# Optimization experiments

Measured on AMD Instinct MI355X. Metric: run time of the kernel, lower is better.

Reference implementation:

```python
import jax, jax.numpy as jnp
import numpy as np

ROPE_DIMS = 16
NUM_HEADS = 16
NUM_KV_HEADS = 4
HEAD_DIM = 128
ROPE_BASE = 10000.0


def _rope_cos_sin(T, dtype):
    # inv_freq over rope_dims=16 -> 8 freqs; emb = cat(freqs, freqs) -> 16 cols
    inv_freq = 1.0 / (ROPE_BASE ** (jnp.arange(0, ROPE_DIMS, 2, dtype=jnp.float32) / ROPE_DIMS))
    t = jnp.arange(T, dtype=jnp.float32)
    freqs = jnp.outer(t, inv_freq)              # [T, 8]
    emb = jnp.concatenate([freqs, freqs], -1)   # [T, 16]
    return jnp.cos(emb).astype(dtype), jnp.sin(emb).astype(dtype)


def _apply_rotary(x):
    # x: [B, H, T, head_dim]; rotate only first ROPE_DIMS dims
    T = x.shape[-2]
    cos, sin = _rope_cos_sin(T, x.dtype)        # [T, 16]
    x_rope, x_pass = x[..., :ROPE_DIMS], x[..., ROPE_DIMS:]
    half = ROPE_DIMS // 2
    x1, x2 = x_rope[..., :half], x_rope[..., half:]
    rotated = jnp.concatenate([-x2, x1], -1)
    x_rope = x_rope * cos + rotated * sin
    return jnp.concatenate([x_rope, x_pass], -1)


def setup_inputs() -> dict:
    key = jax.random.key(0)
    ks = jax.random.split(key, 5)
    B, T, C = 4, 2048, 2048
    kv_out = NUM_KV_HEADS * HEAD_DIM
    s = 0.02
    return {
        "x_normed": jax.random.normal(ks[0], (B, T, C), jnp.float32),
        "q_w": jax.random.normal(ks[1], (C, C), jnp.float32) * s,
        "k_w": jax.random.normal(ks[2], (kv_out, C), jnp.float32) * s,
        "v_w": jax.random.normal(ks[3], (kv_out, C), jnp.float32) * s,
        "out_w": jax.random.normal(ks[4], (C, C), jnp.float32) * s,
        "qk_gain": jnp.ones((1, NUM_HEADS, 1, 1), jnp.float32),
    }


def reference(x_normed, q_w, k_w, v_w, out_w, qk_gain):
    B, T, C = x_normed.shape
    H, kvH, hd = NUM_HEADS, NUM_KV_HEADS, HEAD_DIM
    q = (x_normed @ q_w.T).reshape(B, T, H, hd).transpose(0, 2, 1, 3)    # [B,H,T,hd]
    k = (x_normed @ k_w.T).reshape(B, T, kvH, hd).transpose(0, 2, 1, 3)  # [B,kvH,T,hd]
    v = (x_normed @ v_w.T).reshape(B, T, kvH, hd).transpose(0, 2, 1, 3)
    q = _apply_rotary(q)
    k = _apply_rotary(k)
    q = q * qk_gain
    reps = H // kvH
    if reps > 1:
        k = jnp.repeat(k, reps, axis=1)  # [B,H,T,hd]
        v = jnp.repeat(v, reps, axis=1)
    scale = 1.0 / jnp.sqrt(jnp.asarray(hd, q.dtype))
    scores = jnp.einsum('bhqd,bhkd->bhqk', q, k) * scale
    causal = jnp.tril(jnp.ones((T, T), bool))
    scores = jnp.where(causal, scores, jnp.asarray(-jnp.inf, scores.dtype))
    probs = jax.nn.softmax(scores, axis=-1)
    attn = jnp.einsum('bhqk,bhkd->bhqd', probs, v)
    attn = attn.transpose(0, 2, 1, 3).reshape(B, T, C)
    out = attn @ out_w.T
    return out, v[:, :kvH]
```

## Files before the change

### kernel.cpp

```cpp
#include <hip/hip_runtime.h>
#include <hip/hip_bf16.h>
#include <stdint.h>
#include <math.h>

#define T_SEQ 2048
#define CDIM  2048
#define NB    4
#define NH    16
#define NKV   4
#define HD    128

typedef __attribute__((ext_vector_type(8))) short short8;
typedef __attribute__((ext_vector_type(4))) float f32x4;

__device__ __forceinline__ void gload_lds16(const void* g, void* l) {
  __builtin_amdgcn_global_load_lds((const __attribute__((address_space(1))) void*)g,
                                   (__attribute__((address_space(3))) void*)l, 16, 0, 0);
}

__device__ __forceinline__ f32x4 mfma_bf16(short8 a, short8 b, f32x4 c) {
  return __builtin_amdgcn_mfma_f32_16x16x32_bf16(a, b, c, 0, 0, 0);
}

__device__ __forceinline__ unsigned short f2bf(float x) {
  union { float f; unsigned u; } v; v.f = x;
  unsigned r = v.u + 0x7fffu + ((v.u >> 16) & 1u);
  return (unsigned short)(r >> 16);
}

__device__ __forceinline__ unsigned pk_bf16(float a, float b) {
  unsigned r;
  asm("v_cvt_pk_bf16_f32 %0, %1, %2" : "=v"(r) : "v"(a), "v"(b));
  return r;
}

__device__ __forceinline__ float exp2_fast(float x) {
  float r;
  asm("v_exp_f32 %0, %1" : "=v"(r) : "v"(x));
  return r;
}

__device__ __forceinline__ void barrier_hard() {
  __builtin_amdgcn_s_barrier();
  __builtin_amdgcn_sched_barrier(0);
}

__global__ void cvt_all(const float* __restrict__ x,  const float* __restrict__ qw,
                        const float* __restrict__ kw, const float* __restrict__ vw,
                        const float* __restrict__ ow,
                        unsigned short* __restrict__ xb,  unsigned short* __restrict__ qwb,
                        unsigned short* __restrict__ kwb, unsigned short* __restrict__ vwb,
                        unsigned short* __restrict__ owb) {
  const int bid = blockIdx.x;
  const float* src; unsigned short* dst; int base, nb, n4;
  if (bid < 2048)      { src = x;  dst = xb;  base = 0;    nb = 2048; n4 = 4194304; }
  else if (bid < 2560) { src = qw; dst = qwb; base = 2048; nb = 512;  n4 = 1048576; }
  else if (bid < 2688) { src = kw; dst = kwb; base = 2560; nb = 128;  n4 = 262144;  }
  else if (bid < 2816) { src = vw; dst = vwb; base = 2688; nb = 128;  n4 = 262144;  }
  else                 { src = ow; dst = owb; base = 2816; nb = 512;  n4 = 1048576; }
  const int stride = nb * 256;
  for (int i = (bid - base) * 256 + threadIdx.x; i < n4; i += stride) {
    float4 v = *(const float4*)(src + (size_t)i * 4);
    ushort4 o;
    o.x = f2bf(v.x); o.y = f2bf(v.y); o.z = f2bf(v.z); o.w = f2bf(v.w);
    *(ushort4*)(dst + (size_t)i * 4) = o;
  }
}

template<int MODE>
__launch_bounds__(512, 2)
__global__ void gemm256(const unsigned short* __restrict__ A,
                        const unsigned short* __restrict__ W,
                        int N, int K,
                        unsigned short* __restrict__ obf,
                        float* __restrict__ of32,
                        const float* __restrict__ gain)
{
  __shared__ alignas(16) short As[2][2][256 * 32];
  __shared__ alignas(16) short Bs[2][2][256 * 32];
  const int tid = threadIdx.x;
  const int lane = tid & 63, w = tid >> 6;
  const int wr = w >> 2, wc = w & 3;
  const int lr = lane & 15, lg = lane >> 4;

  const int nwg  = gridDim.x * gridDim.y;
  const int orig = blockIdx.y * gridDim.x + blockIdx.x;
  const int cpx  = nwg >> 3;
  const int swz  = (orig & 7) * cpx + (orig >> 3);
  const int m0 = (swz / gridDim.x) * 256, n0 = (swz % gridDim.x) * 256;

  f32x4 acc[8][4] = {};
  const int nkt = K >> 6;
  const int rsw = (lr >> 1) & 3;

  auto stageA = [&](int kt, int buf, int kk) {
#pragma unroll
    for (int i = 0; i < 2; ++i) {
      int t = i * 512 + tid;
      int row = t >> 2;
      int cs = (t & 3) ^ ((t >> 3) & 3);
      gload_lds16(A + (size_t)(m0 + row) * K + kt * 64 + kk * 32 + cs * 8,
                  (char*)&As[buf][kk][0] + i * 8192 + w * 1024);
    }
  };
  auto stageB = [&](int kt, int buf, int kk) {
#pragma unroll
    for (int i = 0; i < 2; ++i) {
      int t = i * 512 + tid;
      int row = t >> 2;
      int cs = (t & 3) ^ ((t >> 3) & 3);
      gload_lds16(W + (size_t)(n0 + row) * K + kt * 64 + kk * 32 + cs * 8,
                  (char*)&Bs[buf][kk][0] + i * 8192 + w * 1024);
    }
  };

  stageA(0, 0, 0); stageB(0, 0, 0); stageA(0, 0, 1); stageB(0, 0, 1);
  asm volatile("s_waitcnt vmcnt(4)" ::: "memory");
  __builtin_amdgcn_s_barrier();

  int cur = 0;
  for (int kt = 0; kt < nkt; ++kt) {
    const int tn = (kt + 1 < nkt) ? kt + 1 : kt;
#pragma unroll
    for (int kk = 0; kk < 2; ++kk) {
      short8 bfr[4], af[4];
#pragma unroll
      for (int fn = 0; fn < 4; ++fn) {
        int rb = wc * 64 + fn * 16 + lr;
        bfr[fn] = *(const short8*)((const char*)&Bs[cur][kk][0] + rb * 64 + ((lg ^ rsw) << 4));
      }
#pragma unroll
      for (int fm = 0; fm < 4; ++fm) {
        int ra = wr * 128 + fm * 16 + lr;
        af[fm] = *(const short8*)((const char*)&As[cur][kk][0] + ra * 64 + ((lg ^ rsw) << 4));
      }
      stageA(tn, cur ^ 1, kk);
      __builtin_amdgcn_s_barrier();
      __builtin_amdgcn_s_setprio(1);
#pragma unroll
      for (int fm = 0; fm < 4; ++fm)
#pragma unroll
        for (int fn = 0; fn < 4; ++fn)
          acc[fm][fn] = mfma_bf16(af[fm], bfr[fn], acc[fm][fn]);
      __builtin_amdgcn_s_setprio(0);
      __builtin_amdgcn_s_barrier();

#pragma unroll
      for (int fm = 0; fm < 4; ++fm) {
        int ra = wr * 128 + (4 + fm) * 16 + lr;
        af[fm] = *(const short8*)((const char*)&As[cur][kk][0] + ra * 64 + ((lg ^ rsw) << 4));
      }
      stageB(tn, cur ^ 1, kk);
      asm volatile("s_waitcnt vmcnt(4)" ::: "memory");
      __builtin_amdgcn_s_barrier();
      __builtin_amdgcn_s_setprio(1);
#pragma unroll
      for (int fm = 0; fm < 4; ++fm)
#pragma unroll
        for (int fn = 0; fn < 4; ++fn)
          acc[4 + fm][fn] = mfma_bf16(af[fm], bfr[fn], acc[4 + fm][fn]);
      __builtin_amdgcn_s_setprio(0);
      __builtin_amdgcn_s_barrier();
    }
    cur ^= 1;
  }
  asm volatile("s_waitcnt vmcnt(0)" ::: "memory");

#pragma unroll
  for (int fm = 0; fm < 8; ++fm) {
    const int mbase = m0 + wr * 128 + fm * 16 + lg * 4;
#pragma unroll
    for (int fn = 0; fn < 4; ++fn) {
      const int ncol = n0 + wc * 64 + fn * 16 + lr;
      if constexpr (MODE == 0) {
#pragma unroll
        for (int r = 0; r < 4; ++r)
          of32[(size_t)(mbase + r) * N + ncol] = acc[fm][fn][r];
      } else {
        const int hh = ncol >> 7;
        const int d  = ncol & 127;
        const bool rope = ((wc & 1) == 0) && (fn == 0);
#pragma unroll
        for (int r = 0; r < 4; ++r) {
          float val = acc[fm][fn][r];
          const int m  = mbase + r;
          const int t  = m & (T_SEQ - 1);
          const int bb = m >> 11;
          if (rope) {
            float partner = __shfl_xor(val, 8);
            float invf = exp2f(-(float)(d & 7) * 1.6609640474436813f);
            float ang = (float)t * invf;
            float sn, cn;
            sincosf(ang, &sn, &cn);
            float rot = (d < 8) ? -partner : partner;
            val = val * cn + rot * sn;
          }
          val *= gain[hh] * 0.12751742676f;
          obf[(size_t)((bb * NH + hh) * T_SEQ + t) * HD + d] = f2bf(val);
        }
      }
    }
  }
}

__launch_bounds__(256, 2)
__global__ void gemm_kv(const unsigned short* __restrict__ A,
                        const unsigned short* __restrict__ W,
                        unsigned short* __restrict__ Kout,
                        unsigned short* __restrict__ Vt,
                        float* __restrict__ vout)
{
  __shared__ alignas(16) short As[128 * 64];
  __shared__ alignas(16) short Bs[128 * 64];
  __shared__ alignas(16) short Ts[128 * 132];
  const int K = CDIM;
  const int tid = threadIdx.x;
  const int lane = tid & 63, w = tid >> 6;
  const int wr = w >> 1, wc = w & 1;
  const int lr = lane & 15, lg = lane >> 4;

  const int nwg  = gridDim.x * gridDim.y;
  const int orig = blockIdx.y * gridDim.x + blockIdx.x;
  const int cpx  = nwg >> 3;
  const int swz  = (orig & 7) * cpx + (orig >> 3);
  const int m0 = (swz / gridDim.x) * 128, n0 = (swz % gridDim.x) * 128;

  f32x4 acc[4][4] = {};

  const int nkt = K >> 6;
  for (int kt = 0; kt < nkt; ++kt) {
    __syncthreads();
#pragma unroll
    for (int q = 0; q < 4; ++q) {
      int s = (w * 4 + q) * 64 + lane;
      int row = s >> 3;
      int cs2 = (s & 7) ^ (row & 7);
      gload_lds16(A + (size_t)(m0 + row) * K + (kt << 6) + cs2 * 8,
                  (char*)As + (w * 4 + q) * 1024);
      gload_lds16(W + (size_t)(n0 + row) * K + (kt << 6) + cs2 * 8,
                  (char*)Bs + (w * 4 + q) * 1024);
    }
    __syncthreads();
#pragma unroll
    for (int ks = 0; ks < 2; ++ks) {
      short8 af[4], bfr[4];
#pragma unroll
      for (int i = 0; i < 4; ++i) {
        int ra = wr * 64 + i * 16 + lr;
        int rb = wc * 64 + i * 16 + lr;
        af[i]  = *(const short8*)(As + ra * 64 + (((ks * 4 + lg) ^ (ra & 7)) << 3));
        bfr[i] = *(const short8*)(Bs + rb * 64 + (((ks * 4 + lg) ^ (rb & 7)) << 3));
      }
#pragma unroll
      for (int i = 0; i < 4; ++i)
#pragma unroll
        for (int j = 0; j < 4; ++j)
          acc[i][j] = mfma_bf16(af[i], bfr[j], acc[i][j]);
    }
  }

  const int hh = n0 >> 7;
  const int bb = m0 >> 11;
  const int tb = m0 & (T_SEQ - 1);

  if (hh < 4) {
#pragma unroll
    for (int i = 0; i < 4; ++i) {
      const int tl = wr * 64 + i * 16 + lg * 4;
#pragma unroll
      for (int j = 0; j < 4; ++j) {
        const int d = wc * 64 + j * 16 + lr;
        const bool rope = (wc == 0) && (j == 0);
#pragma unroll
        for (int r = 0; r < 4; ++r) {
          float val = acc[i][j][r];
          const int t = tb + tl + r;
          if (rope) {
            float partner = __shfl_xor(val, 8);
            float invf = exp2f(-(float)(d & 7) * 1.6609640474436813f);
            float ang = (float)t * invf;
            float sn, cn;
            sincosf(ang, &sn, &cn);
            float rot = (d < 8) ? -partner : partner;
            val = val * cn + rot * sn;
          }
          Kout[(size_t)((bb * NKV + hh) * T_SEQ + t) * HD + d] = f2bf(val);
        }
      }
    }
  } else {
    const int hv = hh - 4;
#pragma unroll
    for (int i = 0; i < 4; ++i) {
      const int tl = wr * 64 + i * 16 + lg * 4;
#pragma unroll
      for (int j = 0; j < 4; ++j) {
        const int d = wc * 64 + j * 16 + lr;
        if (hv == 0) {
#pragma unroll
          for (int r = 0; r < 4; ++r) {
            float val = acc[i][j][r];
#pragma unroll
            for (int rep = 0; rep < NKV; ++rep)
              vout[(size_t)((bb * NKV + rep) * T_SEQ + tb + tl + r) * HD + d] = val;
          }
        }
        uint2 w2;
        w2.x = pk_bf16(acc[i][j][0], acc[i][j][1]);
        w2.y = pk_bf16(acc[i][j][2], acc[i][j][3]);
        *(uint2*)(Ts + d * 132 + tl) = w2;
      }
    }
    __syncthreads();
    const int d = tid >> 1, off = (tid & 1) * 64;
    unsigned short* dst = Vt + ((size_t)(bb * NKV + hv) * HD + d) * T_SEQ + tb + off;
    const short* srcp = Ts + d * 132 + off;
#pragma unroll
    for (int jj = 0; jj < 8; ++jj)
      *(short8*)(dst + jj * 8) = *(const short8*)(srcp + jj * 8);
  }
}

__launch_bounds__(256, 2)
__global__ void attn_fwd(const unsigned short* __restrict__ Q,
                         const unsigned short* __restrict__ Kg,
                         const unsigned short* __restrict__ Vt,
                         unsigned short* __restrict__ O)
{
  __shared__ alignas(16) short Ks[2][64 * 128];
  __shared__ alignas(16) short Vs[2][128 * 64];
  __shared__ alignas(16) short Ps[128 * 64];

  const int pairi = blockIdx.x;
  const int hp = blockIdx.y, b = blockIdx.z;
  const int kvh = hp >> 1;
  const int h0 = kvh * 4 + (hp & 1) * 2, h1 = h0 + 1;
  const int tid = threadIdx.x, lane = tid & 63, w = tid >> 6;
  const int lr = lane & 15, lg = lane >> 4;

  const unsigned short* Qb0 = Q  + ((size_t)(b * NH  + h0)  * T_SEQ) * HD;
  const unsigned short* Qb1 = Q  + ((size_t)(b * NH  + h1)  * T_SEQ) * HD;
  const unsigned short* Kb  = Kg + ((size_t)(b * NKV + kvh) * T_SEQ) * HD;
  const unsigned short* Vtb = Vt + ((size_t)(b * NKV + kvh) * HD) * T_SEQ;

  auto stageK = [&](int kt, int buf) {
#pragma unroll
    for (int i = 0; i < 4; ++i) {
      int s = i * 256 + tid;
      int row = s >> 4, c = s & 15, cs = c ^ (row & 7);
      gload_lds16(Kb + (size_t)(kt * 64 + row) * HD + cs * 8,
                  (char*)&Ks[buf][0] + i * 4096 + w * 1024);
    }
  };
  auto stageV = [&](int kt, int buf) {
#pragma unroll
    for (int i = 0; i < 4; ++i) {
      int s = i * 256 + tid;
      int row = s >> 3, c = s & 7, cs = c ^ (row & 7);
      gload_lds16(Vtb + (size_t)row * T_SEQ + kt * 64 + cs * 8,
                  (char*)&Vs[buf][0] + i * 4096 + w * 1024);
    }
  };

  auto run_seg = [&](int qtile) {
    const int q0 = qtile * 64;
    const int rw = q0 + w * 16;
    const int qg = rw + lr;

    short8 qf0[4], qf1[4];
#pragma unroll
    for (int ks = 0; ks < 4; ++ks) {
      qf0[ks] = *(const short8*)(Qb0 + (size_t)qg * HD + ks * 32 + lg * 8);
      qf1[ks] = *(const short8*)(Qb1 + (size_t)qg * HD + ks * 32 + lg * 8);
    }

    f32x4 acc0[8] = {}, acc1[8] = {};
    float lrow0 = 0.0f, lrow1 = 0.0f;

    const int nkt = qtile + 1;

    stageK(0, 0);
    stageV(0, 0);
    asm volatile("s_waitcnt vmcnt(4)" ::: "memory");
    barrier_hard();
    int cur = 0;

    const f32x4 minit = {-16.f, -16.f, -16.f, -16.f};

    for (int kt = 0; kt < nkt; ++kt) {
      const int tn = (kt + 1 < nkt) ? kt + 1 : kt;
      stageK(tn, cur ^ 1);

      {
        const short* KL = &Ks[cur][0];
        f32x4 s0[4] = {minit, minit, minit, minit};
        f32x4 s1[4] = {minit, minit, minit, minit};
        __builtin_amdgcn_s_setprio(1);
#pragma unroll
        for (int kb = 0; kb < 4; ++kb) {
          int key = kb * 16 + lr;
#pragma unroll
          for (int ks = 0; ks < 4; ++ks) {
            short8 kf = *(const short8*)(KL + key * 128 + (((ks * 4 + lg) ^ (key & 7)) << 3));
            s0[kb] = mfma_bf16(kf, qf0[ks], s0[kb]);
            s1[kb] = mfma_bf16(kf, qf1[ks], s1[kb]);
          }
        }
        __builtin_amdgcn_s_setprio(0);

        if (kt == qtile) {
#pragma unroll
          for (int kb = 0; kb < 4; ++kb)
#pragma unroll
            for (int r = 0; r < 4; ++r)
              if (kt * 64 + kb * 16 + lg * 4 + r > qg) {
                s0[kb][r] = -3.0e38f;
                s1[kb][r] = -3.0e38f;
              }
        }

        float sum0 = 0.f, sum1 = 0.f;
#pragma unroll
        for (int kb = 0; kb < 4; ++kb) {
          int cc = (kb * 2 + (lg >> 1)) ^ (lr & 7);
          {
            float p0 = exp2_fast(s0[kb][0]);
            float p1 = exp2_fast(s0[kb][1]);
            float p2 = exp2_fast(s0[kb][2]);
            float p3 = exp2_fast(s0[kb][3]);
            sum0 += (p0 + p1) + (p2 + p3);
            uint2 w2;
            w2.x = pk_bf16(p0, p1);
            w2.y = pk_bf16(p2, p3);
            *(uint2*)(Ps + (w * 16 + lr) * 64 + (cc << 3) + ((lg & 1) << 2)) = w2;
          }
          {
            float p0 = exp2_fast(s1[kb][0]);
            float p1 = exp2_fast(s1[kb][1]);
            float p2 = exp2_fast(s1[kb][2]);
            float p3 = exp2_fast(s1[kb][3]);
            sum1 += (p0 + p1) + (p2 + p3);
            uint2 w2;
            w2.x = pk_bf16(p0, p1);
            w2.y = pk_bf16(p2, p3);
            *(uint2*)(Ps + (64 + w * 16 + lr) * 64 + (cc << 3) + ((lg & 1) << 2)) = w2;
          }
        }
        lrow0 += sum0;
        lrow1 += sum1;
      }

      stageV(tn, cur ^ 1);
      asm volatile("s_waitcnt vmcnt(8)" ::: "memory");
      barrier_hard();

      {
        const short* VL = &Vs[cur][0];
        const int r0 = w * 16 + lr, r1 = 64 + w * 16 + lr;
        short8 pf00 = *(const short8*)(Ps + r0 * 64 + (((0 + lg) ^ (lr & 7)) << 3));
        short8 pf01 = *(const short8*)(Ps + r0 * 64 + (((4 + lg) ^ (lr & 7)) << 3));
        short8 pf10 = *(const short8*)(Ps + r1 * 64 + (((0 + lg) ^ (lr & 7)) << 3));
        short8 pf11 = *(const short8*)(Ps + r1 * 64 + (((4 + lg) ^ (lr & 7)) << 3));
        __builtin_amdgcn_s_setprio(1);
#pragma unroll
        for (int db = 0; db < 8; ++db) {
          int vrow = db * 16 + lr;
          short8 v0 = *(const short8*)(VL + vrow * 64 + (((0 + lg) ^ (vrow & 7)) << 3));
          short8 v1 = *(const short8*)(VL + vrow * 64 + (((4 + lg) ^ (vrow & 7)) << 3));
          acc0[db] = mfma_bf16(v0, pf00, acc0[db]);
          acc0[db] = mfma_bf16(v1, pf01, acc0[db]);
          acc1[db] = mfma_bf16(v0, pf10, acc1[db]);
          acc1[db] = mfma_bf16(v1, pf11, acc1[db]);
        }
        __builtin_amdgcn_s_setprio(0);
      }

      asm volatile("s_waitcnt vmcnt(4)" ::: "memory");
      barrier_hard();
      cur ^= 1;
    }

    asm volatile("s_waitcnt vmcnt(0)" ::: "memory");
    barrier_hard();

    lrow0 += __shfl_xor(lrow0, 16); lrow0 += __shfl_xor(lrow0, 32);
    lrow1 += __shfl_xor(lrow1, 16); lrow1 += __shfl_xor(lrow1, 32);
    float inv0 = 1.0f / lrow0, inv1 = 1.0f / lrow1;
#pragma unroll
    for (int db = 0; db < 8; ++db) {
      uint2 o2;
      o2.x = pk_bf16(acc0[db][0] * inv0, acc0[db][1] * inv0);
      o2.y = pk_bf16(acc0[db][2] * inv0, acc0[db][3] * inv0);
      *(uint2*)(O + (size_t)(b * T_SEQ + qg) * CDIM + h0 * HD + db * 16 + lg * 4) = o2;
      uint2 o3;
      o3.x = pk_bf16(acc1[db][0] * inv1, acc1[db][1] * inv1);
      o3.y = pk_bf16(acc1[db][2] * inv1, acc1[db][3] * inv1);
      *(uint2*)(O + (size_t)(b * T_SEQ + qg) * CDIM + h1 * HD + db * 16 + lg * 4) = o3;
    }
  };

  run_seg(31 - pairi);
  run_seg(pairi);
}

extern "C" void kernel_launch(void* const* d_in, const int* in_sizes, int n_in,
                              void* d_out, int out_size, void* d_ws, size_t ws_size,
                              hipStream_t stream) {
  (void)in_sizes; (void)n_in; (void)out_size; (void)ws_size;
  const float* x    = (const float*)d_in[0];
  const float* qw   = (const float*)d_in[1];
  const float* kw   = (const float*)d_in[2];
  const float* vw   = (const float*)d_in[3];
  const float* ow   = (const float*)d_in[4];
  const float* gain = (const float*)d_in[5];
  float* out  = (float*)d_out;
  float* vout = out + (size_t)NB * T_SEQ * CDIM;

  char* ws = (char*)d_ws;
  unsigned short* xb  = (unsigned short*)(ws);
  unsigned short* Qb  = (unsigned short*)(ws + 33554432);
  unsigned short* Kb  = (unsigned short*)(ws + 67108864);
  unsigned short* qwb = (unsigned short*)(ws + 83886080);
  unsigned short* kwb = (unsigned short*)(ws + 92274688);
  unsigned short* vwb = (unsigned short*)(ws + 94371840);
  unsigned short* owb = (unsigned short*)(ws + 96468992);
  unsigned short* Ab  = xb;
  unsigned short* Vtb = qwb;

  cvt_all<<<3328, 256, 0, stream>>>(x, qw, kw, vw, ow, xb, qwb, kwb, vwb, owb);

  gemm256<1><<<dim3(8, 32), 512, 0, stream>>>(xb, qwb, CDIM, CDIM, Qb, nullptr, gain);
  gemm_kv<<<dim3(8, 64), 256, 0, stream>>>(xb, kwb, Kb, Vtb, vout);

  attn_fwd<<<dim3(16, 8, 4), 256, 0, stream>>>(Qb, Kb, Vtb, Ab);

  gemm256<0><<<dim3(8, 32), 512, 0, stream>>>(Ab, owb, CDIM, CDIM, nullptr, out, nullptr);
}
```

Before: 292.9 us.

## Halve attention KV tile to 32 keys, one q-tile per block, raise occupancy

```diff
diff --git a/kernel.cpp b/kernel.cpp
--- a/kernel.cpp
+++ b/kernel.cpp
@@ -321,17 +321,18 @@
   }
 }
 
-__launch_bounds__(256, 2)
+__launch_bounds__(256, 4)
 __global__ void attn_fwd(const unsigned short* __restrict__ Q,
                          const unsigned short* __restrict__ Kg,
                          const unsigned short* __restrict__ Vt,
                          unsigned short* __restrict__ O)
 {
-  __shared__ alignas(16) short Ks[2][64 * 128];
-  __shared__ alignas(16) short Vs[2][128 * 64];
-  __shared__ alignas(16) short Ps[128 * 64];
-
-  const int pairi = blockIdx.x;
+  __shared__ alignas(16) short Ks[2][32 * 128];
+  __shared__ alignas(16) short Vs[2][128 * 32];
+  __shared__ alignas(16) short Ps[128 * 32];
+
+  const int bx = blockIdx.x;
+  const int qtile = (bx & 1) ? (31 - (bx >> 1)) : (bx >> 1);
   const int hp = blockIdx.y, b = blockIdx.z;
   const int kvh = hp >> 1;
   const int h0 = kvh * 4 + (hp & 1) * 2, h1 = h0 + 1;
@@ -345,162 +346,151 @@
 
   auto stageK = [&](int kt, int buf) {
 #pragma unroll
-    for (int i = 0; i < 4; ++i) {
+    for (int i = 0; i < 2; ++i) {
       int s = i * 256 + tid;
       int row = s >> 4, c = s & 15, cs = c ^ (row & 7);
-      gload_lds16(Kb + (size_t)(kt * 64 + row) * HD + cs * 8,
+      gload_lds16(Kb + (size_t)(kt * 32 + row) * HD + cs * 8,
                   (char*)&Ks[buf][0] + i * 4096 + w * 1024);
     }
   };
   auto stageV = [&](int kt, int buf) {
 #pragma unroll
-    for (int i = 0; i < 4; ++i) {
+    for (int i = 0; i < 2; ++i) {
       int s = i * 256 + tid;
-      int row = s >> 3, c = s & 7, cs = c ^ (row & 7);
-      gload_lds16(Vtb + (size_t)row * T_SEQ + kt * 64 + cs * 8,
+      int row = s >> 2, c = s & 3, cs = c ^ (row & 3);
+      gload_lds16(Vtb + (size_t)row * T_SEQ + kt * 32 + cs * 8,
                   (char*)&Vs[buf][0] + i * 4096 + w * 1024);
     }
   };
 
-  auto run_seg = [&](int qtile) {
-    const int q0 = qtile * 64;
-    const int rw = q0 + w * 16;
-    const int qg = rw + lr;
-
-    short8 qf0[4], qf1[4];
-#pragma unroll
-    for (int ks = 0; ks < 4; ++ks) {
-      qf0[ks] = *(const short8*)(Qb0 + (size_t)qg * HD + ks * 32 + lg * 8);
-      qf1[ks] = *(const short8*)(Qb1 + (size_t)qg * HD + ks * 32 + lg * 8);
-    }
-
-    f32x4 acc0[8] = {}, acc1[8] = {};
-    float lrow0 = 0.0f, lrow1 = 0.0f;
-
-    const int nkt = qtile + 1;
-
-    stageK(0, 0);
-    stageV(0, 0);
+  const int rw = qtile * 64 + w * 16;
+  const int qg = rw + lr;
+
+  short8 qf0[4], qf1[4];
+#pragma unroll
+  for (int ks = 0; ks < 4; ++ks) {
+    qf0[ks] = *(const short8*)(Qb0 + (size_t)qg * HD + ks * 32 + lg * 8);
+    qf1[ks] = *(const short8*)(Qb1 + (size_t)qg * HD + ks * 32 + lg * 8);
+  }
+
+  f32x4 acc0[8] = {}, acc1[8] = {};
+  float lrow0 = 0.0f, lrow1 = 0.0f;
+
+  const int nkt = 2 * qtile + 2;
+
+  stageK(0, 0);
+  stageV(0, 0);
+  asm volatile("s_waitcnt vmcnt(2)" ::: "memory");
+  barrier_hard();
+  int cur = 0;
+
+  const f32x4 minit = {-16.f, -16.f, -16.f, -16.f};
+
+  for (int kt = 0; kt < nkt; ++kt) {
+    const int tn = (kt + 1 < nkt) ? kt + 1 : kt;
+    stageK(tn, cur ^ 1);
+
+    {
+      const short* KL = &Ks[cur][0];
+      f32x4 s0[2] = {minit, minit};
+      f32x4 s1[2] = {minit, minit};
+      __builtin_amdgcn_s_setprio(1);
+#pragma unroll
+      for (int kb = 0; kb < 2; ++kb) {
+        int key = kb * 16 + lr;
+#pragma unroll
+        for (int ks = 0; ks < 4; ++ks) {
+          short8 kf = *(const short8*)(KL + key * 128 + (((ks * 4 + lg) ^ (key & 7)) << 3));
+          s0[kb] = mfma_bf16(kf, qf0[ks], s0[kb]);
+          s1[kb] = mfma_bf16(kf, qf1[ks], s1[kb]);
+        }
+      }
+      __builtin_amdgcn_s_setprio(0);
+
+      if (kt * 32 + 31 > rw) {
+#pragma unroll
+        for (int kb = 0; kb < 2; ++kb)
+#pragma unroll
+          for (int r = 0; r < 4; ++r)
+            if (kt * 32 + kb * 16 + lg * 4 + r > qg) {
+              s0[kb][r] = -3.0e38f;
+              s1[kb][r] = -3.0e38f;
+            }
+      }
+
+      float sum0 = 0.f, sum1 = 0.f;
+#pragma unroll
+      for (int kb = 0; kb < 2; ++kb) {
+        int cc = (kb * 2 + (lg >> 1)) ^ (lr & 3);
+        {
+          float p0 = exp2_fast(s0[kb][0]);
+          float p1 = exp2_fast(s0[kb][1]);
+          float p2 = exp2_fast(s0[kb][2]);
+          float p3 = exp2_fast(s0[kb][3]);
+          sum0 += (p0 + p1) + (p2 + p3);
+          uint2 w2;
+          w2.x = pk_bf16(p0, p1);
+          w2.y = pk_bf16(p2, p3);
+          *(uint2*)(Ps + (w * 16 + lr) * 32 + (cc << 3) + ((lg & 1) << 2)) = w2;
+        }
+        {
+          float p0 = exp2_fast(s1[kb][0]);
+          float p1 = exp2_fast(s1[kb][1]);
+          float p2 = exp2_fast(s1[kb][2]);
+          float p3 = exp2_fast(s1[kb][3]);
+          sum1 += (p0 + p1) + (p2 + p3);
+          uint2 w2;
+          w2.x = pk_bf16(p0, p1);
+          w2.y = pk_bf16(p2, p3);
+          *(uint2*)(Ps + (64 + w * 16 + lr) * 32 + (cc << 3) + ((lg & 1) << 2)) = w2;
+        }
+      }
+      lrow0 += sum0;
+      lrow1 += sum1;
+    }
+
+    stageV(tn, cur ^ 1);
     asm volatile("s_waitcnt vmcnt(4)" ::: "memory");
     barrier_hard();
-    int cur = 0;
-
-    const f32x4 minit = {-16.f, -16.f, -16.f, -16.f};
-
-    for (int kt = 0; kt < nkt; ++kt) {
-      const int tn = (kt + 1 < nkt) ? kt + 1 : kt;
-      stageK(tn, cur ^ 1);
-
-      {
-        const short* KL = &Ks[cur][0];
-        f32x4 s0[4] = {minit, minit, minit, minit};
-        f32x4 s1[4] = {minit, minit, minit, minit};
-        __builtin_amdgcn_s_setprio(1);
-#pragma unroll
-        for (int kb = 0; kb < 4; ++kb) {
-          int key = kb * 16 + lr;
-#pragma unroll
-          for (int ks = 0; ks < 4; ++ks) {
-            short8 kf = *(const short8*)(KL + key * 128 + (((ks * 4 + lg) ^ (key & 7)) << 3));
-            s0[kb] = mfma_bf16(kf, qf0[ks], s0[kb]);
-            s1[kb] = mfma_bf16(kf, qf1[ks], s1[kb]);
-          }
-        }
-        __builtin_amdgcn_s_setprio(0);
-
-        if (kt == qtile) {
-#pragma unroll
-          for (int kb = 0; kb < 4; ++kb)
-#pragma unroll
-            for (int r = 0; r < 4; ++r)
-              if (kt * 64 + kb * 16 + lg * 4 + r > qg) {
-                s0[kb][r] = -3.0e38f;
-                s1[kb][r] = -3.0e38f;
-              }
-        }
-
-        float sum0 = 0.f, sum1 = 0.f;
-#pragma unroll
-        for (int kb = 0; kb < 4; ++kb) {
-          int cc = (kb * 2 + (lg >> 1)) ^ (lr & 7);
-          {
-            float p0 = exp2_fast(s0[kb][0]);
-            float p1 = exp2_fast(s0[kb][1]);
-            float p2 = exp2_fast(s0[kb][2]);
-            float p3 = exp2_fast(s0[kb][3]);
-            sum0 += (p0 + p1) + (p2 + p3);
-            uint2 w2;
-            w2.x = pk_bf16(p0, p1);
-            w2.y = pk_bf16(p2, p3);
-            *(uint2*)(Ps + (w * 16 + lr) * 64 + (cc << 3) + ((lg & 1) << 2)) = w2;
-          }
-          {
-            float p0 = exp2_fast(s1[kb][0]);
-            float p1 = exp2_fast(s1[kb][1]);
-            float p2 = exp2_fast(s1[kb][2]);
-            float p3 = exp2_fast(s1[kb][3]);
-            sum1 += (p0 + p1) + (p2 + p3);
-            uint2 w2;
-            w2.x = pk_bf16(p0, p1);
-            w2.y = pk_bf16(p2, p3);
-            *(uint2*)(Ps + (64 + w * 16 + lr) * 64 + (cc << 3) + ((lg & 1) << 2)) = w2;
-          }
-        }
-        lrow0 += sum0;
-        lrow1 += sum1;
-      }
-
-      stageV(tn, cur ^ 1);
-      asm volatile("s_waitcnt vmcnt(8)" ::: "memory");
-      barrier_hard();
-
-      {
-        const short* VL = &Vs[cur][0];
-        const int r0 = w * 16 + lr, r1 = 64 + w * 16 + lr;
-        short8 pf00 = *(const short8*)(Ps + r0 * 64 + (((0 + lg) ^ (lr & 7)) << 3));
-        short8 pf01 = *(const short8*)(Ps + r0 * 64 + (((4 + lg) ^ (lr & 7)) << 3));
-        short8 pf10 = *(const short8*)(Ps + r1 * 64 + (((0 + lg) ^ (lr & 7)) << 3));
-        short8 pf11 = *(const short8*)(Ps + r1 * 64 + (((4 + lg) ^ (lr & 7)) << 3));
-        __builtin_amdgcn_s_setprio(1);
-#pragma unroll
-        for (int db = 0; db < 8; ++db) {
-          int vrow = db * 16 + lr;
-          short8 v0 = *(const short8*)(VL + vrow * 64 + (((0 + lg) ^ (vrow & 7)) << 3));
-          short8 v1 = *(const short8*)(VL + vrow * 64 + (((4 + lg) ^ (vrow & 7)) << 3));
-          acc0[db] = mfma_bf16(v0, pf00, acc0[db]);
-          acc0[db] = mfma_bf16(v1, pf01, acc0[db]);
-          acc1[db] = mfma_bf16(v0, pf10, acc1[db]);
-          acc1[db] = mfma_bf16(v1, pf11, acc1[db]);
-        }
-        __builtin_amdgcn_s_setprio(0);
-      }
-
-      asm volatile("s_waitcnt vmcnt(4)" ::: "memory");
-      barrier_hard();
-      cur ^= 1;
-    }
-
-    asm volatile("s_waitcnt vmcnt(0)" ::: "memory");
+
+    {
+      const short* VL = &Vs[cur][0];
+      const int r0 = w * 16 + lr, r1 = 64 + w * 16 + lr;
+      short8 pf0 = *(const short8*)(Ps + r0 * 32 + ((lg ^ (lr & 3)) << 3));
+      short8 pf1 = *(const short8*)(Ps + r1 * 32 + ((lg ^ (lr & 3)) << 3));
+      __builtin_amdgcn_s_setprio(1);
+#pragma unroll
+      for (int db = 0; db < 8; ++db) {
+        int vrow = db * 16 + lr;
+        short8 vf = *(const short8*)(VL + vrow * 32 + ((lg ^ (vrow & 3)) << 3));
+        acc0[db] = mfma_bf16(vf, pf0, acc0[db]);
+        acc1[db] = mfma_bf16(vf, pf1, acc1[db]);
+      }
+      __builtin_amdgcn_s_setprio(0);
+    }
+
+    asm volatile("s_waitcnt vmcnt(2)" ::: "memory");
     barrier_hard();
-
-    lrow0 += __shfl_xor(lrow0, 16); lrow0 += __shfl_xor(lrow0, 32);
-    lrow1 += __shfl_xor(lrow1, 16); lrow1 += __shfl_xor(lrow1, 32);
-    float inv0 = 1.0f / lrow0, inv1 = 1.0f / lrow1;
-#pragma unroll
-    for (int db = 0; db < 8; ++db) {
-      uint2 o2;
-      o2.x = pk_bf16(acc0[db][0] * inv0, acc0[db][1] * inv0);
-      o2.y = pk_bf16(acc0[db][2] * inv0, acc0[db][3] * inv0);
-      *(uint2*)(O + (size_t)(b * T_SEQ + qg) * CDIM + h0 * HD + db * 16 + lg * 4) = o2;
-      uint2 o3;
-      o3.x = pk_bf16(acc1[db][0] * inv1, acc1[db][1] * inv1);
-      o3.y = pk_bf16(acc1[db][2] * inv1, acc1[db][3] * inv1);
-      *(uint2*)(O + (size_t)(b * T_SEQ + qg) * CDIM + h1 * HD + db * 16 + lg * 4) = o3;
-    }
-  };
-
-  run_seg(31 - pairi);
-  run_seg(pairi);
+    cur ^= 1;
+  }
+
+  asm volatile("s_waitcnt vmcnt(0)" ::: "memory");
+  barrier_hard();
+
+  lrow0 += __shfl_xor(lrow0, 16); lrow0 += __shfl_xor(lrow0, 32);
+  lrow1 += __shfl_xor(lrow1, 16); lrow1 += __shfl_xor(lrow1, 32);
+  float inv0 = 1.0f / lrow0, inv1 = 1.0f / lrow1;
+#pragma unroll
+  for (int db = 0; db < 8; ++db) {
+    uint2 o2;
+    o2.x = pk_bf16(acc0[db][0] * inv0, acc0[db][1] * inv0);
+    o2.y = pk_bf16(acc0[db][2] * inv0, acc0[db][3] * inv0);
+    *(uint2*)(O + (size_t)(b * T_SEQ + qg) * CDIM + h0 * HD + db * 16 + lg * 4) = o2;
+    uint2 o3;
+    o3.x = pk_bf16(acc1[db][0] * inv1, acc1[db][1] * inv1);
+    o3.y = pk_bf16(acc1[db][2] * inv1, acc1[db][3] * inv1);
+    *(uint2*)(O + (size_t)(b * T_SEQ + qg) * CDIM + h1 * HD + db * 16 + lg * 4) = o3;
+  }
 }
 
 extern "C" void kernel_launch(void* const* d_in, const int* in_sizes, int n_in,
@@ -532,7 +522,7 @@
   gemm256<1><<<dim3(8, 32), 512, 0, stream>>>(xb, qwb, CDIM, CDIM, Qb, nullptr, gain);
   gemm_kv<<<dim3(8, 64), 256, 0, stream>>>(xb, kwb, Kb, Vtb, vout);
 
-  attn_fwd<<<dim3(16, 8, 4), 256, 0, stream>>>(Qb, Kb, Vtb, Ab);
+  attn_fwd<<<dim3(32, 8, 4), 256, 0, stream>>>(Qb, Kb, Vtb, Ab);
 
   gemm256<0><<<dim3(8, 32), 512, 0, stream>>>(Ab, owb, CDIM, CDIM, nullptr, out, nullptr);
 }
```

Measured after the change: 547.2 us. 1.87x slower.
